# Performance work log

Measured on AMD Instinct MI355X. Metric: run time of the kernel, lower is better.

## Reference

```python
import jax, jax.numpy as jnp
import numpy as np

B, S, E = 4, 2048, 1024
H, D, F = 16, 64, 4096
EPS = 1e-5


def layer_norm(x, gamma, beta):
    mu = jnp.mean(x, axis=-1, keepdims=True)
    var = jnp.mean(jnp.square(x - mu), axis=-1, keepdims=True)
    return (x - mu) * jax.lax.rsqrt(var + EPS) * gamma + beta


def setup_inputs() -> dict:
    key = jax.random.key(0)
    ks = jax.random.split(key, 8)
    scale = 0.02  # keep logits in a numerically sane range
    X = jax.random.normal(ks[0], (B, S, E), dtype=jnp.float32)
    WQ = jax.random.normal(ks[1], (H, E, D), dtype=jnp.float32) * scale
    WK = jax.random.normal(ks[2], (H, E, D), dtype=jnp.float32) * scale
    WV = jax.random.normal(ks[3], (H, E, D), dtype=jnp.float32) * scale
    WO = jax.random.normal(ks[4], (H * D, E), dtype=jnp.float32) * scale
    gamma = jnp.ones((E,), dtype=jnp.float32)
    beta = jnp.zeros((E,), dtype=jnp.float32)
    W1 = jax.random.normal(ks[5], (E, F), dtype=jnp.float32) * scale
    b1 = jnp.zeros((F,), dtype=jnp.float32)
    W2 = jax.random.normal(ks[6], (F, E), dtype=jnp.float32) * scale
    b2 = jnp.zeros((E,), dtype=jnp.float32)
    return {"X": X, "WQ": WQ, "WK": WK, "WV": WV, "WO": WO,
            "gamma": gamma, "beta": beta, "W1": W1, "b1": b1, "W2": W2, "b2": b2}


def reference(X, WQ, WK, WV, WO, gamma, beta, W1, b1, W2, b2):
    # Batched-over-heads version of the per-head python loop (same math).
    Q = jnp.einsum('bse,hed->bhsd', X, WQ)  # [B,H,S,D]
    K = jnp.einsum('bse,hed->bhsd', X, WK)
    V = jnp.einsum('bse,hed->bhsd', X, WV)
    scores = jnp.einsum('bhsd,bhtd->bhst', Q, K)  # [B,H,S,T]
    # FAITHFUL quirk: torch.softmax(..., dim=1) on a [B,S,S] tensor normalizes
    # over the QUERY axis (axis=2 here), then divides by sqrt(D) AFTER softmax.
    att = jax.nn.softmax(scores, axis=2) / jnp.sqrt(jnp.float32(D))
    vec = jnp.einsum('bhst,bhtd->bhsd', att, V)  # [B,H,S,D]
    att_vec = jnp.transpose(vec, (0, 2, 1, 3)).reshape(X.shape[0], X.shape[1], H * D)
    vector_att = layer_norm(att_vec @ WO + X, gamma, beta)
    vector_ffn = jax.nn.relu(vector_att @ W1 + b1) @ W2 + b2
    return layer_norm(vector_ffn + vector_att, gamma, beta)
```

## Files before the change

### kernel.cpp

```cpp
#include <hip/hip_runtime.h>
#include <cstddef>
#include <cstdint>

#define BB 4
#define SS 2048
#define EE 1024
#define HH 16
#define DD 64
#define FF 4096

typedef unsigned short u16;
typedef __attribute__((ext_vector_type(8))) short short8;
typedef __attribute__((ext_vector_type(4))) short short4v;
typedef __attribute__((ext_vector_type(16))) float f32x16;
typedef __attribute__((ext_vector_type(4))) unsigned u32x4;

__device__ __forceinline__ u16 f2bf(float x) {
    unsigned u = __builtin_bit_cast(unsigned, x);
    u += 0x7fffu + ((u >> 16) & 1u);
    return (u16)(u >> 16);
}
__device__ __forceinline__ float bf2f(u16 h) {
    unsigned u = ((unsigned)h) << 16;
    return __builtin_bit_cast(float, u);
}
__device__ __forceinline__ float ex2(float x) {
    float r;
    asm("v_exp_f32 %0, %1" : "=v"(r) : "v"(x));
    return r;
}
__device__ __forceinline__ unsigned cvtpk(float lo, float hi) {
    unsigned r;
    asm("v_cvt_pk_bf16_f32 %0, %1, %2" : "=v"(r) : "v"(lo), "v"(hi));
    return r;
}
__device__ __forceinline__ void pl32swap2(unsigned &a, unsigned &b,
                                          unsigned &c, unsigned &d) {
    asm("s_nop 1\n\t"
        "v_permlane32_swap_b32 %0, %1\n\t"
        "v_permlane32_swap_b32 %2, %3\n\t"
        "s_nop 1"
        : "+v"(a), "+v"(b), "+v"(c), "+v"(d));
}
__device__ __forceinline__ int sw(int row, int lbyte) {
    return row * 128 + (lbyte ^ ((row & 7) << 4));
}

#define GLD_LDS16(g, l)                                                     \
    __builtin_amdgcn_global_load_lds(                                       \
        (const __attribute__((address_space(1))) void*)(g),                 \
        (__attribute__((address_space(3))) void*)(l), 16, 0, 0)

__global__ __launch_bounds__(256) void cvt_bf(const float* __restrict__ in,
                                              u16* __restrict__ out, int n4) {
    const int i = blockIdx.x * 256 + threadIdx.x;
    if (i < n4) {
        float4 v = reinterpret_cast<const float4*>(in)[i];
        short4v o;
        o.x = (short)f2bf(v.x); o.y = (short)f2bf(v.y);
        o.z = (short)f2bf(v.z); o.w = (short)f2bf(v.w);
        reinterpret_cast<short4v*>(out)[i] = o;
    }
}

__global__ __launch_bounds__(256) void transp_bf(const float* __restrict__ in,
                                                 u16* __restrict__ out, int R, int C) {
    __shared__ float T[64][65];
    const int r0 = blockIdx.x * 64, c0 = blockIdx.y * 64;
    const size_t zoff = (size_t)blockIdx.z * R * C;
    in += zoff; out += zoff;
    const int tid = threadIdx.x;
#pragma unroll 4
    for (int i = 0; i < 16; ++i) {
        int l = tid + i * 256;
        T[l >> 6][l & 63] = in[(size_t)(r0 + (l >> 6)) * C + c0 + (l & 63)];
    }
    __syncthreads();
#pragma unroll 4
    for (int i = 0; i < 16; ++i) {
        int l = tid + i * 256;
        out[(size_t)(c0 + (l >> 6)) * R + r0 + (l & 63)] = f2bf(T[l & 63][l >> 6]);
    }
}

#define WAITV6 asm volatile("s_waitcnt vmcnt(6)" ::: "memory")
#define WAITV0 asm volatile("s_waitcnt vmcnt(0)" ::: "memory")

#define STAGE(p, k0u)                                                         \
    do {                                                                      \
        _Pragma("unroll")                                                     \
        for (int i_ = 0; i_ < 4; ++i_)                                        \
            GLD_LDS16(Ag + (size_t)(i_ * 64) * K + (k0u),                     \
                      &lds[(p) * 24576 + (i_ * 64 + w * 8) * 64]);            \
        _Pragma("unroll")                                                     \
        for (int j_ = 0; j_ < 2; ++j_)                                        \
            GLD_LDS16(Bg + (size_t)(j_ * 64) * K + (k0u),                     \
                      &lds[(p) * 24576 + 16384 + (j_ * 64 + w * 8) * 64]);    \
    } while (0)

template <int EPI>
__global__ __launch_bounds__(512, 2) void gemm256(const u16* __restrict__ A,
                                                  const u16* __restrict__ BT,
                                                  int K, int N, int gy,
                                                  void* __restrict__ Cout,
                                                  const float* __restrict__ bias,
                                                  const void* __restrict__ resid,
                                                  float oscale,
                                                  void* __restrict__ Cout2) {
    __shared__ __align__(16) u16 lds[2 * 24576];
    const int nwg = gridDim.x;
    const int bid = blockIdx.x;
    const int qq = nwg >> 3, rr = nwg & 7;
    const int xcd = bid & 7, lin = bid >> 3;
    const int wgid = (xcd < rr ? xcd * (qq + 1) : rr * (qq + 1) + (xcd - rr) * qq) + lin;
    const int x = wgid / gy, y = wgid % gy;
    const int m0 = x * 256, n0 = y * 128;

    const int tid = threadIdx.x;
    const int w = tid >> 6, l = tid & 63;
    const int l32 = l & 31, hf = l >> 5;
    const int wm = w >> 1, wn = w & 1;

    const int swz = ((l & 7) ^ (l >> 3)) * 8;
    const u16* Ag = A + (size_t)(m0 + w * 8 + (l >> 3)) * K + swz;
    const u16* Bg = BT + (size_t)(n0 + w * 8 + (l >> 3)) * K + swz;

    const int NTt = K >> 6;
    f32x16 acc[2][2] = {};

    STAGE(0, 0);
    STAGE(1, 64);

    for (int t = 0; t < NTt; ++t) {
        const int p = t & 1;
        if (t < NTt - 1) { WAITV6; } else { WAITV0; }
        __builtin_amdgcn_sched_barrier(0);
        __builtin_amdgcn_s_barrier();
        __builtin_amdgcn_sched_barrier(0);
        __builtin_amdgcn_s_setprio(1);
        const u16* Ab = &lds[p * 24576];
        const u16* Bb = &lds[p * 24576 + 16384];
#pragma unroll
        for (int kt = 0; kt < 4; ++kt) {
            const int cs = (((kt * 2 + hf) ^ (l32 & 7)) * 8);
            short8 af[2], bfr[2];
#pragma unroll
            for (int mb = 0; mb < 2; ++mb)
                af[mb] = *(const short8*)&Ab[(wm * 64 + mb * 32 + l32) * 64 + cs];
#pragma unroll
            for (int nb = 0; nb < 2; ++nb)
                bfr[nb] = *(const short8*)&Bb[(wn * 64 + nb * 32 + l32) * 64 + cs];
#pragma unroll
            for (int mb = 0; mb < 2; ++mb)
#pragma unroll
                for (int nb = 0; nb < 2; ++nb)
                    acc[mb][nb] = __builtin_amdgcn_mfma_f32_32x32x16_bf16(af[mb], bfr[nb], acc[mb][nb], 0, 0, 0);
        }
        __builtin_amdgcn_s_setprio(0);
        __builtin_amdgcn_sched_barrier(0);
        __builtin_amdgcn_s_barrier();
        __builtin_amdgcn_sched_barrier(0);
        if (t + 2 < NTt) STAGE(p, (t + 2) * 64);
    }

    u16* dst4 = nullptr;
    float sc4 = 1.0f;
    if (EPI == 4) {
        const bool isK = (n0 >= 1024);
        dst4 = isK ? (u16*)Cout2 : (u16*)Cout;
        sc4 = isK ? 1.0f : oscale;
    }

#pragma unroll
    for (int mb = 0; mb < 2; ++mb)
#pragma unroll
        for (int nb = 0; nb < 2; ++nb) {
            const int col = n0 + wn * 64 + nb * 32 + l32;
#pragma unroll
            for (int r = 0; r < 16; ++r) {
                const int row = m0 + wm * 64 + mb * 32 + (r & 3) + 8 * (r >> 2) + 4 * hf;
                float v = acc[mb][nb][r];
                const size_t idx = (size_t)row * N + col;
                if (EPI == 0) {
                    ((u16*)Cout)[idx] = f2bf(v * oscale);
                } else if (EPI == 1) {
                    ((float*)Cout)[idx] = v + ((const float*)resid)[idx];
                } else if (EPI == 2) {
                    v += bias[col];
                    ((u16*)Cout)[idx] = f2bf(fmaxf(v, 0.f));
                } else if (EPI == 3) {
                    v += bias[col] + bf2f(((const u16*)resid)[idx]);
                    ((float*)Cout)[idx] = v;
                } else {
                    dst4[(size_t)row * 1024 + (col & 1023)] = f2bf(v * sc4);
                }
            }
        }
}

__global__ __launch_bounds__(256) void stats32(const u16* __restrict__ Qg,
                                               const u16* __restrict__ Kg,
                                               u16* __restrict__ Vtg) {
    __shared__ u16 Qs[2][64 * 64];
    __shared__ float lbuf[128];
    const int bid = blockIdx.x;
    const int wgid = (bid & 7) * 128 + (bid >> 3);
    const int t0 = (wgid & 15) * 128;
    const int bh = wgid >> 4;
    const int b = bh >> 4, h = bh & 15;
    const int tid = threadIdx.x;
    const int w = tid >> 6, l = tid & 63;
    const int l32 = l & 31, hf = l >> 5;
    const u16* Qp = Qg + (size_t)b * SS * 1024 + h * 64;
    const u16* Kp = Kg + (size_t)b * SS * 1024 + h * 64;
    const int sr = tid >> 3, dg = (tid & 7) * 8;

    short8 kf[4];
#pragma unroll
    for (int ks = 0; ks < 4; ++ks)
        kf[ks] = *(const short8*)(Kp + (size_t)(t0 + w * 32 + l32) * 1024 + ks * 16 + hf * 8);

    short8 pq0 = *(const short8*)(Qp + (size_t)sr * 1024 + dg);
    short8 pq1 = *(const short8*)(Qp + (size_t)(sr + 32) * 1024 + dg);
    *(short8*)((char*)Qs[0] + sw(sr, dg * 2)) = pq0;
    *(short8*)((char*)Qs[0] + sw(sr + 32, dg * 2)) = pq1;
    pq0 = *(const short8*)(Qp + (size_t)(64 + sr) * 1024 + dg);
    pq1 = *(const short8*)(Qp + (size_t)(64 + sr + 32) * 1024 + dg);
    __syncthreads();

    float ls0 = 0.f, ls1 = 0.f;
    for (int st = 0; st < 32; ++st) {
        const int p = st & 1;
        if (st + 1 < 32) {
            *(short8*)((char*)Qs[p ^ 1] + sw(sr, dg * 2)) = pq0;
            *(short8*)((char*)Qs[p ^ 1] + sw(sr + 32, dg * 2)) = pq1;
        }
        if (st + 2 < 32) {
            const int s1 = (st + 2) * 64;
            pq0 = *(const short8*)(Qp + (size_t)(s1 + sr) * 1024 + dg);
            pq1 = *(const short8*)(Qp + (size_t)(s1 + sr + 32) * 1024 + dg);
        }
        f32x16 sc0 = {}, sc1 = {};
        __builtin_amdgcn_s_setprio(1);
#pragma unroll
        for (int ks = 0; ks < 4; ++ks) {
            short8 a0 = *(const short8*)((char*)Qs[p] + sw(l32, ks * 32 + hf * 16));
            short8 a1 = *(const short8*)((char*)Qs[p] + sw(32 + l32, ks * 32 + hf * 16));
            sc0 = __builtin_amdgcn_mfma_f32_32x32x16_bf16(a0, kf[ks], sc0, 0, 0, 0);
            sc1 = __builtin_amdgcn_mfma_f32_32x32x16_bf16(a1, kf[ks], sc1, 0, 0, 0);
        }
        __builtin_amdgcn_s_setprio(0);
#pragma unroll
        for (int r = 0; r < 16; ++r) { ls0 += ex2(sc0[r]); ls1 += ex2(sc1[r]); }
        __syncthreads();
    }
    float lsum = ls0 + ls1;
    lsum += __shfl_xor(lsum, 32);
    if (hf == 0) lbuf[w * 32 + l32] = 0.125f / lsum;
    __syncthreads();

    const int d = tid >> 2, cb = (tid & 3) * 32;
    u16* vp = Vtg + (size_t)(h * 64 + d) * 8192 + b * SS + t0 + cb;
#pragma unroll
    for (int j = 0; j < 4; ++j) {
        short8 v = *(short8*)(vp + j * 8);
        short8 o;
#pragma unroll
        for (int i = 0; i < 8; ++i)
            o[i] = (short)f2bf(bf2f((u16)v[i]) * lbuf[cb + j * 8 + i]);
        *(short8*)(vp + j * 8) = o;
    }
}

__global__ __launch_bounds__(256) void pv_fused(const u16* __restrict__ Qg,
                                                const u16* __restrict__ Kg,
                                                const u16* __restrict__ Vtg,
                                                u16* __restrict__ vecbf) {
    __shared__ u16 Ks[2][64 * 64];
    __shared__ u16 Vs[2][64 * 64];
    const int bid = blockIdx.x;
    const int wgid = (bid & 7) * 128 + (bid >> 3);
    const int s0 = (wgid & 15) * 128;
    const int bh = wgid >> 4;
    const int b = bh >> 4, h = bh & 15;
    const int tid = threadIdx.x;
    const int w = tid >> 6, l = tid & 63;
    const int l32 = l & 31, hf = l >> 5;
    const u16* Qp = Qg + (size_t)b * SS * 1024 + h * 64;
    const u16* Kp = Kg + (size_t)b * SS * 1024 + h * 64;
    const u16* Vp = Vtg + (size_t)h * 64 * 8192 + (size_t)b * SS;
    const int sr = tid >> 3, dg = (tid & 7) * 8;

    short8 qf[4];
#pragma unroll
    for (int ks = 0; ks < 4; ++ks)
        qf[ks] = *(const short8*)(Qp + (size_t)(s0 + w * 32 + l32) * 1024 + ks * 16 + hf * 8);

    short8 pk0 = *(const short8*)(Kp + (size_t)sr * 1024 + dg);
    short8 pk1 = *(const short8*)(Kp + (size_t)(sr + 32) * 1024 + dg);
    short8 pv0 = *(const short8*)(Vp + (size_t)sr * 8192 + dg);
    short8 pv1 = *(const short8*)(Vp + (size_t)(sr + 32) * 8192 + dg);
    *(short8*)((char*)Ks[0] + sw(sr, dg * 2)) = pk0;
    *(short8*)((char*)Ks[0] + sw(sr + 32, dg * 2)) = pk1;
    *(short8*)((char*)Vs[0] + sw(sr, dg * 2)) = pv0;
    *(short8*)((char*)Vs[0] + sw(sr + 32, dg * 2)) = pv1;
    pk0 = *(const short8*)(Kp + (size_t)(64 + sr) * 1024 + dg);
    pk1 = *(const short8*)(Kp + (size_t)(64 + sr + 32) * 1024 + dg);
    pv0 = *(const short8*)(Vp + (size_t)sr * 8192 + 64 + dg);
    pv1 = *(const short8*)(Vp + (size_t)(sr + 32) * 8192 + 64 + dg);
    __syncthreads();

    f32x16 acc[2] = {};
    for (int tt = 0; tt < 32; ++tt) {
        const int p = tt & 1;
        if (tt + 1 < 32) {
            *(short8*)((char*)Ks[p ^ 1] + sw(sr, dg * 2)) = pk0;
            *(short8*)((char*)Ks[p ^ 1] + sw(sr + 32, dg * 2)) = pk1;
            *(short8*)((char*)Vs[p ^ 1] + sw(sr, dg * 2)) = pv0;
            *(short8*)((char*)Vs[p ^ 1] + sw(sr + 32, dg * 2)) = pv1;
        }
        if (tt + 2 < 32) {
            const int t1 = (tt + 2) * 64;
            pk0 = *(const short8*)(Kp + (size_t)(t1 + sr) * 1024 + dg);
            pk1 = *(const short8*)(Kp + (size_t)(t1 + sr + 32) * 1024 + dg);
            pv0 = *(const short8*)(Vp + (size_t)sr * 8192 + t1 + dg);
            pv1 = *(const short8*)(Vp + (size_t)(sr + 32) * 8192 + t1 + dg);
        }
        f32x16 sc0 = {}, sc1 = {};
        __builtin_amdgcn_s_setprio(1);
#pragma unroll
        for (int ks = 0; ks < 4; ++ks) {
            short8 a0 = *(const short8*)((char*)Ks[p] + sw(l32, ks * 32 + hf * 16));
            short8 a1 = *(const short8*)((char*)Ks[p] + sw(32 + l32, ks * 32 + hf * 16));
            sc0 = __builtin_amdgcn_mfma_f32_32x32x16_bf16(a0, qf[ks], sc0, 0, 0, 0);
            sc1 = __builtin_amdgcn_mfma_f32_32x32x16_bf16(a1, qf[ks], sc1, 0, 0, 0);
        }
        __builtin_amdgcn_s_setprio(0);
        unsigned cp0[8], cp1[8];
#pragma unroll
        for (int p2 = 0; p2 < 8; ++p2) {
            cp0[p2] = cvtpk(ex2(sc0[2 * p2]), ex2(sc0[2 * p2 + 1]));
            cp1[p2] = cvtpk(ex2(sc1[2 * p2]), ex2(sc1[2 * p2 + 1]));
        }
        short8 pa[4];
#pragma unroll
        for (int ks2 = 0; ks2 < 4; ++ks2) {
            unsigned* cp = (ks2 & 2) ? cp1 : cp0;
            const int c = (ks2 & 1) * 4;
            unsigned w0 = cp[c + 0], w2 = cp[c + 2];
            unsigned w1 = cp[c + 1], w3 = cp[c + 3];
            pl32swap2(w0, w2, w1, w3);
            u32x4 t4; t4.x = w0; t4.y = w1; t4.z = w2; t4.w = w3;
            pa[ks2] = __builtin_bit_cast(short8, t4);
        }
        __builtin_amdgcn_s_setprio(1);
#pragma unroll
        for (int ks2 = 0; ks2 < 4; ++ks2)
#pragma unroll
            for (int nf = 0; nf < 2; ++nf) {
                short8 bfr = *(const short8*)((char*)Vs[p] + sw(nf * 32 + l32, ks2 * 32 + hf * 16));
                acc[nf] = __builtin_amdgcn_mfma_f32_32x32x16_bf16(pa[ks2], bfr, acc[nf], 0, 0, 0);
            }
        __builtin_amdgcn_s_setprio(0);
        __syncthreads();
    }
#pragma unroll
    for (int nf = 0; nf < 2; ++nf) {
        const int col = h * 64 + nf * 32 + l32;
#pragma unroll
        for (int r = 0; r < 16; ++r) {
            const int srow = s0 + w * 32 + (r & 3) + 8 * (r >> 2) + 4 * hf;
            vecbf[(size_t)(b * SS + srow) * 1024 + col] = f2bf(acc[nf][r]);
        }
    }
}

__global__ __launch_bounds__(256) void ln_bf_kernel(const float* __restrict__ buf,
                                                    const float* __restrict__ g,
                                                    const float* __restrict__ be,
                                                    u16* __restrict__ outbf) {
    const int row = blockIdx.x;
    const int tid = threadIdx.x;
    const float* p = buf + (size_t)row * EE;
    float4 x = reinterpret_cast<const float4*>(p)[tid];
    float s = x.x + x.y + x.z + x.w;
    __shared__ float red[4];
#pragma unroll
    for (int o = 32; o > 0; o >>= 1) s += __shfl_down(s, o);
    const int wid = tid >> 6, lane = tid & 63;
    if (lane == 0) red[wid] = s;
    __syncthreads();
    const float mu = (red[0] + red[1] + red[2] + red[3]) * (1.0f / EE);
    __syncthreads();
    const float dx = x.x - mu, dy = x.y - mu, dz = x.z - mu, dw = x.w - mu;
    float v = dx * dx + dy * dy + dz * dz + dw * dw;
#pragma unroll
    for (int o = 32; o > 0; o >>= 1) v += __shfl_down(v, o);
    if (lane == 0) red[wid] = v;
    __syncthreads();
    const float var = (red[0] + red[1] + red[2] + red[3]) * (1.0f / EE);
    const float rs = rsqrtf(var + 1e-5f);
    float4 gv = reinterpret_cast<const float4*>(g)[tid];
    float4 bv = reinterpret_cast<const float4*>(be)[tid];
    short4v o;
    o.x = (short)f2bf(dx * rs * gv.x + bv.x);
    o.y = (short)f2bf(dy * rs * gv.y + bv.y);
    o.z = (short)f2bf(dz * rs * gv.z + bv.z);
    o.w = (short)f2bf(dw * rs * gv.w + bv.w);
    reinterpret_cast<short4v*>(outbf + (size_t)row * EE)[tid] = o;
}

__global__ __launch_bounds__(256) void ln_kernel(float* __restrict__ buf,
                                                 const float* __restrict__ g,
                                                 const float* __restrict__ be) {
    const int row = blockIdx.x;
    const int tid = threadIdx.x;
    float* p = buf + (size_t)row * EE;
    float4 x = reinterpret_cast<float4*>(p)[tid];
    float s = x.x + x.y + x.z + x.w;
    __shared__ float red[4];
#pragma unroll
    for (int o = 32; o > 0; o >>= 1) s += __shfl_down(s, o);
    const int wid = tid >> 6, lane = tid & 63;
    if (lane == 0) red[wid] = s;
    __syncthreads();
    const float mu = (red[0] + red[1] + red[2] + red[3]) * (1.0f / EE);
    __syncthreads();
    const float dx = x.x - mu, dy = x.y - mu, dz = x.z - mu, dw = x.w - mu;
    float v = dx * dx + dy * dy + dz * dz + dw * dw;
#pragma unroll
    for (int o = 32; o > 0; o >>= 1) v += __shfl_down(v, o);
    if (lane == 0) red[wid] = v;
    __syncthreads();
    const float var = (red[0] + red[1] + red[2] + red[3]) * (1.0f / EE);
    const float rs = rsqrtf(var + 1e-5f);
    float4 gv = reinterpret_cast<const float4*>(g)[tid];
    float4 bv = reinterpret_cast<const float4*>(be)[tid];
    float4 y;
    y.x = dx * rs * gv.x + bv.x;
    y.y = dy * rs * gv.y + bv.y;
    y.z = dz * rs * gv.z + bv.z;
    y.w = dw * rs * gv.w + bv.w;
    reinterpret_cast<float4*>(p)[tid] = y;
}

extern "C" void kernel_launch(void* const* d_in, const int* in_sizes, int n_in,
                              void* d_out, int out_size, void* d_ws, size_t ws_size,
                              hipStream_t stream) {
    const float* X     = (const float*)d_in[0];
    const float* WQ    = (const float*)d_in[1];
    const float* WK    = (const float*)d_in[2];
    const float* WV    = (const float*)d_in[3];
    const float* WO    = (const float*)d_in[4];
    const float* gamma = (const float*)d_in[5];
    const float* beta  = (const float*)d_in[6];
    const float* W1    = (const float*)d_in[7];
    const float* b1    = (const float*)d_in[8];
    const float* W2    = (const float*)d_in[9];
    const float* b2    = (const float*)d_in[10];
    float* out = (float*)d_out;

    char* ws = (char*)d_ws;
    const size_t MB = 1024 * 1024;
    u16* WQT   = (u16*)(ws + 0);
    u16* WKT   = (u16*)(ws + 2 * MB);
    u16* WVT   = (u16*)(ws + 4 * MB);
    u16* WOT   = (u16*)(ws + 6 * MB);
    u16* W1T   = (u16*)(ws + 8 * MB);
    u16* W2T   = (u16*)(ws + 16 * MB);
    u16* Qbf   = (u16*)(ws + 25 * MB);
    u16* Kbf   = (u16*)(ws + 41 * MB);
    u16* Vt    = (u16*)(ws + 57 * MB);
    u16* vecbf = (u16*)(ws + 73 * MB);
    u16* hid   = (u16*)(ws + 25 * MB);
    u16* Xbf   = (u16*)(ws + 89 * MB);
    float* vatt  = (float*)(ws + 105 * MB);
    u16*   ln1bf = (u16*)(ws + 137 * MB);

    const int NT = BB * SS;

    cvt_bf<<<8192, 256, 0, stream>>>(X, Xbf, NT * EE / 4);
    transp_bf<<<dim3(16, 1, 16), 256, 0, stream>>>(WQ, WQT, EE, DD);
    transp_bf<<<dim3(16, 1, 16), 256, 0, stream>>>(WK, WKT, EE, DD);
    transp_bf<<<dim3(16, 1, 16), 256, 0, stream>>>(WV, WVT, EE, DD);
    transp_bf<<<dim3(16, 16, 1), 256, 0, stream>>>(WO, WOT, HH * DD, EE);
    transp_bf<<<dim3(16, 64, 1), 256, 0, stream>>>(W1, W1T, EE, FF);
    transp_bf<<<dim3(64, 16, 1), 256, 0, stream>>>(W2, W2T, FF, EE);

    gemm256<4><<<512, 512, 0, stream>>>(Xbf, WQT, 1024, 2048, 16, Qbf, nullptr, nullptr, 1.44269504089f, Kbf);
    gemm256<0><<<256, 512, 0, stream>>>(WVT, Xbf, 1024, 8192, 64, Vt, nullptr, nullptr, 1.0f, nullptr);

    stats32<<<1024, 256, 0, stream>>>(Qbf, Kbf, Vt);
    pv_fused<<<1024, 256, 0, stream>>>(Qbf, Kbf, Vt, vecbf);

    gemm256<1><<<256, 512, 0, stream>>>(vecbf, WOT, 1024, 1024, 8, vatt, nullptr, X, 1.0f, nullptr);
    ln_bf_kernel<<<NT, 256, 0, stream>>>(vatt, gamma, beta, ln1bf);

    gemm256<2><<<1024, 512, 0, stream>>>(ln1bf, W1T, 1024, FF, 32, hid, b1, nullptr, 1.0f, nullptr);
    gemm256<3><<<256, 512, 0, stream>>>(hid, W2T, FF, 1024, 8, out, b2, ln1bf, 1.0f, nullptr);

    ln_kernel<<<NT, 256, 0, stream>>>(out, gamma, beta);
}
```

Measured before the change: 584.0 us.

## Double query rows per workgroup in fused PV attention kernel

```diff
diff --git a/kernel.cpp b/kernel.cpp
--- a/kernel.cpp
+++ b/kernel.cpp
@@ -279,9 +279,9 @@
     __shared__ u16 Ks[2][64 * 64];
     __shared__ u16 Vs[2][64 * 64];
     const int bid = blockIdx.x;
-    const int wgid = (bid & 7) * 128 + (bid >> 3);
-    const int s0 = (wgid & 15) * 128;
-    const int bh = wgid >> 4;
+    const int wgid = (bid & 7) * 64 + (bid >> 3);
+    const int s0 = (wgid & 7) * 256;
+    const int bh = wgid >> 3;
     const int b = bh >> 4, h = bh & 15;
     const int tid = threadIdx.x;
     const int w = tid >> 6, l = tid & 63;
@@ -291,10 +291,12 @@
     const u16* Vp = Vtg + (size_t)h * 64 * 8192 + (size_t)b * SS;
     const int sr = tid >> 3, dg = (tid & 7) * 8;
 
-    short8 qf[4];
-#pragma unroll
-    for (int ks = 0; ks < 4; ++ks)
-        qf[ks] = *(const short8*)(Qp + (size_t)(s0 + w * 32 + l32) * 1024 + ks * 16 + hf * 8);
+    short8 qfA[4], qfB[4];
+#pragma unroll
+    for (int ks = 0; ks < 4; ++ks) {
+        qfA[ks] = *(const short8*)(Qp + (size_t)(s0 + w * 32 + l32) * 1024 + ks * 16 + hf * 8);
+        qfB[ks] = *(const short8*)(Qp + (size_t)(s0 + 128 + w * 32 + l32) * 1024 + ks * 16 + hf * 8);
+    }
 
     short8 pk0 = *(const short8*)(Kp + (size_t)sr * 1024 + dg);
     short8 pk1 = *(const short8*)(Kp + (size_t)(sr + 32) * 1024 + dg);
@@ -310,7 +312,7 @@
     pv1 = *(const short8*)(Vp + (size_t)(sr + 32) * 8192 + 64 + dg);
     __syncthreads();
 
-    f32x16 acc[2] = {};
+    f32x16 accA[2] = {}, accB[2] = {};
     for (int tt = 0; tt < 32; ++tt) {
         const int p = tt & 1;
         if (tt + 1 < 32) {
@@ -326,42 +328,51 @@
             pv0 = *(const short8*)(Vp + (size_t)sr * 8192 + t1 + dg);
             pv1 = *(const short8*)(Vp + (size_t)(sr + 32) * 8192 + t1 + dg);
         }
-        f32x16 sc0 = {}, sc1 = {};
-        __builtin_amdgcn_s_setprio(1);
-#pragma unroll
-        for (int ks = 0; ks < 4; ++ks) {
-            short8 a0 = *(const short8*)((char*)Ks[p] + sw(l32, ks * 32 + hf * 16));
-            short8 a1 = *(const short8*)((char*)Ks[p] + sw(32 + l32, ks * 32 + hf * 16));
-            sc0 = __builtin_amdgcn_mfma_f32_32x32x16_bf16(a0, qf[ks], sc0, 0, 0, 0);
-            sc1 = __builtin_amdgcn_mfma_f32_32x32x16_bf16(a1, qf[ks], sc1, 0, 0, 0);
-        }
-        __builtin_amdgcn_s_setprio(0);
-        unsigned cp0[8], cp1[8];
-#pragma unroll
-        for (int p2 = 0; p2 < 8; ++p2) {
-            cp0[p2] = cvtpk(ex2(sc0[2 * p2]), ex2(sc0[2 * p2 + 1]));
-            cp1[p2] = cvtpk(ex2(sc1[2 * p2]), ex2(sc1[2 * p2 + 1]));
-        }
-        short8 pa[4];
-#pragma unroll
-        for (int ks2 = 0; ks2 < 4; ++ks2) {
-            unsigned* cp = (ks2 & 2) ? cp1 : cp0;
-            const int c = (ks2 & 1) * 4;
-            unsigned w0 = cp[c + 0], w2 = cp[c + 2];
-            unsigned w1 = cp[c + 1], w3 = cp[c + 3];
-            pl32swap2(w0, w2, w1, w3);
-            u32x4 t4; t4.x = w0; t4.y = w1; t4.z = w2; t4.w = w3;
-            pa[ks2] = __builtin_bit_cast(short8, t4);
-        }
-        __builtin_amdgcn_s_setprio(1);
-#pragma unroll
-        for (int ks2 = 0; ks2 < 4; ++ks2)
-#pragma unroll
-            for (int nf = 0; nf < 2; ++nf) {
-                short8 bfr = *(const short8*)((char*)Vs[p] + sw(nf * 32 + l32, ks2 * 32 + hf * 16));
-                acc[nf] = __builtin_amdgcn_mfma_f32_32x32x16_bf16(pa[ks2], bfr, acc[nf], 0, 0, 0);
+#pragma unroll
+        for (int th = 0; th < 2; ++th) {
+            f32x16 scA = {}, scB = {};
+            __builtin_amdgcn_s_setprio(1);
+#pragma unroll
+            for (int ks = 0; ks < 4; ++ks) {
+                short8 a0 = *(const short8*)((char*)Ks[p] + sw(th * 32 + l32, ks * 32 + hf * 16));
+                scA = __builtin_amdgcn_mfma_f32_32x32x16_bf16(a0, qfA[ks], scA, 0, 0, 0);
+                scB = __builtin_amdgcn_mfma_f32_32x32x16_bf16(a0, qfB[ks], scB, 0, 0, 0);
             }
-        __builtin_amdgcn_s_setprio(0);
+            __builtin_amdgcn_s_setprio(0);
+            unsigned cpA[8], cpB[8];
+#pragma unroll
+            for (int p2 = 0; p2 < 8; ++p2) {
+                cpA[p2] = cvtpk(ex2(scA[2 * p2]), ex2(scA[2 * p2 + 1]));
+                cpB[p2] = cvtpk(ex2(scB[2 * p2]), ex2(scB[2 * p2 + 1]));
+            }
+            short8 paA[2], paB[2];
+#pragma unroll
+            for (int q = 0; q < 2; ++q) {
+                const int c = q * 4;
+                unsigned a0w = cpA[c + 0], a2w = cpA[c + 2];
+                unsigned a1w = cpA[c + 1], a3w = cpA[c + 3];
+                pl32swap2(a0w, a2w, a1w, a3w);
+                u32x4 tA; tA.x = a0w; tA.y = a1w; tA.z = a2w; tA.w = a3w;
+                paA[q] = __builtin_bit_cast(short8, tA);
+                unsigned b0w = cpB[c + 0], b2w = cpB[c + 2];
+                unsigned b1w = cpB[c + 1], b3w = cpB[c + 3];
+                pl32swap2(b0w, b2w, b1w, b3w);
+                u32x4 tB; tB.x = b0w; tB.y = b1w; tB.z = b2w; tB.w = b3w;
+                paB[q] = __builtin_bit_cast(short8, tB);
+            }
+            __builtin_amdgcn_s_setprio(1);
+#pragma unroll
+            for (int q = 0; q < 2; ++q) {
+                const int ks2 = th * 2 + q;
+#pragma unroll
+                for (int nf = 0; nf < 2; ++nf) {
+                    short8 bfr = *(const short8*)((char*)Vs[p] + sw(nf * 32 + l32, ks2 * 32 + hf * 16));
+                    accA[nf] = __builtin_amdgcn_mfma_f32_32x32x16_bf16(paA[q], bfr, accA[nf], 0, 0, 0);
+                    accB[nf] = __builtin_amdgcn_mfma_f32_32x32x16_bf16(paB[q], bfr, accB[nf], 0, 0, 0);
+                }
+            }
+            __builtin_amdgcn_s_setprio(0);
+        }
         __syncthreads();
     }
 #pragma unroll
@@ -369,8 +380,11 @@
         const int col = h * 64 + nf * 32 + l32;
 #pragma unroll
         for (int r = 0; r < 16; ++r) {
-            const int srow = s0 + w * 32 + (r & 3) + 8 * (r >> 2) + 4 * hf;
-            vecbf[(size_t)(b * SS + srow) * 1024 + col] = f2bf(acc[nf][r]);
+            const int ro = (r & 3) + 8 * (r >> 2) + 4 * hf;
+            const int srowA = s0 + w * 32 + ro;
+            vecbf[(size_t)(b * SS + srowA) * 1024 + col] = f2bf(accA[nf][r]);
+            const int srowB = s0 + 128 + w * 32 + ro;
+            vecbf[(size_t)(b * SS + srowB) * 1024 + col] = f2bf(accB[nf][r]);
         }
     }
 }
@@ -491,7 +505,7 @@
     gemm256<0><<<256, 512, 0, stream>>>(WVT, Xbf, 1024, 8192, 64, Vt, nullptr, nullptr, 1.0f, nullptr);
 
     stats32<<<1024, 256, 0, stream>>>(Qbf, Kbf, Vt);
-    pv_fused<<<1024, 256, 0, stream>>>(Qbf, Kbf, Vt, vecbf);
+    pv_fused<<<512, 256, 0, stream>>>(Qbf, Kbf, Vt, vecbf);
 
     gemm256<1><<<256, 512, 0, stream>>>(vecbf, WOT, 1024, 1024, 8, vatt, nullptr, X, 1.0f, nullptr);
     ln_bf_kernel<<<NT, 256, 0, stream>>>(vatt, gamma, beta, ln1bf);
```

Measured after the change: 560.3 us. -4.1%, faster.
